# Kernel optimization log

Measured on AMD Instinct MI355X. Metric: run time of the kernel, lower is better.

Reference implementation:

```python
import jax, jax.numpy as jnp
import numpy as np

N_NODES = 100000
N_EDGES = 640000
N_GRAPHS = 2048
HID = 128
L = 3


def setup_inputs() -> dict:
    key = jax.random.key(0)
    ks = jax.random.split(key, 24)
    f32 = jnp.float32
    x = jax.random.normal(ks[0], (N_NODES, 7), dtype=f32)
    edge_attr = jax.random.normal(ks[1], (N_EDGES, 3), dtype=f32)
    edge_index = jax.random.randint(ks[2], (2, N_EDGES), 0, N_NODES, dtype=jnp.int32)
    batch = jnp.sort(jax.random.randint(ks[3], (N_NODES,), 0, N_GRAPHS, dtype=jnp.int32))

    def lin(k, fi, fo):
        return jax.random.normal(k, (fi, fo), dtype=f32) / jnp.sqrt(jnp.asarray(fi, f32))

    inp = dict(x=x, edge_attr=edge_attr, edge_index=edge_index, batch=batch)
    inp["node_w"] = lin(ks[4], 7, HID); inp["node_b"] = jnp.zeros((HID,), f32)
    inp["ew1"] = lin(ks[5], 3, HID);   inp["eb1"] = jnp.zeros((HID,), f32)
    inp["ew2"] = lin(ks[6], HID, HID); inp["eb2"] = jnp.zeros((HID,), f32)
    inp["cw1"] = jnp.stack([lin(ks[7 + i], HID, HID) for i in range(L)])
    inp["cb1"] = jnp.zeros((L, HID), f32)
    inp["cw2"] = jnp.stack([lin(ks[10 + i], HID, HID) for i in range(L)])
    inp["cb2"] = jnp.zeros((L, HID), f32)
    inp["clw1"] = lin(ks[13], HID, 64); inp["clb1"] = jnp.zeros((64,), f32)
    inp["clw2"] = lin(ks[14], 64, 1);   inp["clb2"] = jnp.zeros((1,), f32)
    inp["rw1"] = lin(ks[15], HID, 64);  inp["rb1"] = jnp.zeros((64,), f32)
    inp["rw2"] = lin(ks[16], 64, 1);    inp["rb2"] = jnp.zeros((1,), f32)
    return inp


def reference(x, edge_attr, node_w, node_b, ew1, eb1, ew2, eb2,
              cw1, cb1, cw2, cb2, clw1, clb1, clw2, clb2,
              rw1, rb1, rw2, rb2, edge_index, batch):
    relu = jax.nn.relu
    # encoders
    h = x @ node_w + node_b                                   # [N, H]
    e = relu(edge_attr @ ew1 + eb1) @ ew2 + eb2               # [E, H]
    src, dst = edge_index[0], edge_index[1]
    for l in range(L):
        # GINEConv (eps=0): out = MLP(h_i + sum_j ReLU(h_j + e_ji))
        m = relu(h[src] + e)                                  # [E, H] gather + edge add
        agg = jax.ops.segment_sum(m, dst, num_segments=N_NODES)
        z = h + agg
        h = relu(z @ cw1[l] + cb1[l]) @ cw2[l] + cb2[l]
        h = relu(h)                                           # dropout = identity (eval)
    # global mean pool
    ones = jnp.ones((h.shape[0],), h.dtype)
    counts = jax.ops.segment_sum(ones, batch, num_segments=N_GRAPHS)
    g = jax.ops.segment_sum(h, batch, num_segments=N_GRAPHS) / jnp.maximum(counts, 1.0)[:, None]
    success_logit = (relu(g @ clw1 + clb1) @ clw2 + clb2)[:, 0]
    route_length = (relu(g @ rw1 + rb1) @ rw2 + rb2)[:, 0]
    return success_logit, route_length
```

## Files before the change

### kernel.cpp

```cpp
#include <hip/hip_runtime.h>

#define HID 128
#define LDP 136

typedef short s16x8 __attribute__((ext_vector_type(8)));
typedef float f32x4 __attribute__((ext_vector_type(4)));

__device__ __forceinline__ float bf2f(unsigned int u) {
  union { unsigned int i; float f; } v; v.i = u << 16; return v.f;
}
__device__ __forceinline__ float asf(unsigned int u) {
  union { unsigned int i; float f; } v; v.i = u; return v.f;
}
__device__ __forceinline__ unsigned short f2bf(float f) {
  union { float f; unsigned int i; } v; v.f = f;
  unsigned int r = v.i + 0x7fffu + ((v.i >> 16) & 1u);
  return (unsigned short)(r >> 16);
}

__global__ void k_zero4(float4* __restrict__ p, size_t n4) {
  size_t i = (size_t)blockIdx.x * blockDim.x + threadIdx.x;
  if (i < n4) p[i] = (float4){0.f, 0.f, 0.f, 0.f};
}

__global__ void k_hist(const int* __restrict__ dst, int* __restrict__ deg, int nE) {
  int e = blockIdx.x * blockDim.x + threadIdx.x;
  if (e < nE) atomicAdd(&deg[dst[e]], 1);
}

__global__ void k_scanA(const int* __restrict__ deg, int* __restrict__ bsum) {
  __shared__ int ss[256];
  int t = threadIdx.x;
  ss[t] = deg[blockIdx.x * 256 + t];
  __syncthreads();
  for (int off = 128; off; off >>= 1) {
    if (t < off) ss[t] += ss[t + off];
    __syncthreads();
  }
  if (t == 0) bsum[blockIdx.x] = ss[0];
}

__global__ void k_scanB(const int* __restrict__ bsum, int* __restrict__ bsumx, int NB) {
  __shared__ int sd[512];
  int t = threadIdx.x;
  int v = (t < NB) ? bsum[t] : 0;
  sd[t] = v;
  __syncthreads();
  for (int off = 1; off < 512; off <<= 1) {
    int a = (t >= off) ? sd[t - off] : 0;
    __syncthreads();
    sd[t] += a;
    __syncthreads();
  }
  if (t < NB) bsumx[t] = sd[t] - v;
}

__global__ void k_scanC(const int* __restrict__ deg, const int* __restrict__ bsumx,
                        int* __restrict__ cursor, int* __restrict__ rowptr) {
  __shared__ int ss[256];
  int t = threadIdx.x, i = blockIdx.x * 256 + t;
  int v = deg[i];
  ss[t] = v;
  __syncthreads();
  for (int off = 1; off < 256; off <<= 1) {
    int a = (t >= off) ? ss[t - off] : 0;
    __syncthreads();
    ss[t] += a;
    __syncthreads();
  }
  int ex = ss[t] - v + bsumx[blockIdx.x];
  cursor[i] = ex;
  rowptr[i] = ex;
}

__global__ void k_scatter(const int* __restrict__ src, const int* __restrict__ dst,
                          const float* __restrict__ ea, int* __restrict__ cursor,
                          int* __restrict__ src_s, float* __restrict__ ea_s, int nE) {
  int e = blockIdx.x * blockDim.x + threadIdx.x;
  if (e >= nE) return;
  int d = dst[e];
  int pos = atomicAdd(&cursor[d], 1);
  src_s[pos] = src[e];
  ea_s[(size_t)pos * 3 + 0] = ea[(size_t)e * 3 + 0];
  ea_s[(size_t)pos * 3 + 1] = ea[(size_t)e * 3 + 1];
  ea_s[(size_t)pos * 3 + 2] = ea[(size_t)e * 3 + 2];
}

__global__ void k_prep_w(const float* __restrict__ ew2, const float* __restrict__ cw1,
                         const float* __restrict__ cw2, unsigned short* __restrict__ wT) {
  int idx = blockIdx.x * blockDim.x + threadIdx.x;
  if (idx >= 7 * 16384) return;
  int m = idx >> 14, i = idx & 16383;
  int n = i >> 7, k = i & 127;
  const float* s = (m == 0) ? ew2 : (m <= 3 ? cw1 + (size_t)(m - 1) * 16384
                                            : cw2 + (size_t)(m - 4) * 16384);
  wT[idx] = f2bf(s[k * 128 + n]);
}

__global__ void k_node_enc(const float* __restrict__ x, const float* __restrict__ w,
                           const float* __restrict__ b, unsigned short* __restrict__ h16, int nN) {
  int idx = blockIdx.x * blockDim.x + threadIdx.x;
  if (idx >= nN * HID) return;
  int i = idx >> 7, j = idx & 127;
  float acc = b[j];
  const float* xr = x + (size_t)i * 7;
#pragma unroll
  for (int k = 0; k < 7; ++k) acc += xr[k] * w[k * HID + j];
  h16[idx] = f2bf(acc);
}

__global__ void __launch_bounds__(256) k_edge_gemm(
    const float* __restrict__ ea_s, const float* __restrict__ ew1, const float* __restrict__ eb1,
    const unsigned short* __restrict__ w2t, const float* __restrict__ eb2,
    unsigned short* __restrict__ e16, int nE) {
  __shared__ __attribute__((aligned(16))) unsigned short ts1[128 * LDP];
  __shared__ float eaL[384];
  int tid = threadIdx.x;
  int e0 = blockIdx.x * 128;
  for (int i = tid; i < 384; i += 256) eaL[i] = ea_s[(size_t)e0 * 3 + i];
  __syncthreads();
  {
    int j = tid & 127, r0 = (tid >> 7) * 64;
    float wa = ew1[j], wb = ew1[HID + j], wc = ew1[2 * HID + j], bj = eb1[j];
    for (int r = r0; r < r0 + 64; ++r) {
      float a = bj + eaL[r * 3] * wa + eaL[r * 3 + 1] * wb + eaL[r * 3 + 2] * wc;
      ts1[r * LDP + j] = f2bf(fmaxf(a, 0.f));
    }
  }
  __syncthreads();
  int wave = tid >> 6, lane = tid & 63;
  int l15 = lane & 15, quad = lane >> 4;
  int rbase = (wave >> 1) * 64, nbase = (wave & 1) * 64;
  f32x4 acc[4][4];
#pragma unroll
  for (int i = 0; i < 4; ++i)
#pragma unroll
    for (int j = 0; j < 4; ++j) acc[i][j] = (f32x4){0.f, 0.f, 0.f, 0.f};
  for (int kc = 0; kc < 4; ++kc) {
    int k0 = kc * 32 + quad * 8;
    s16x8 af[4], bf[4];
#pragma unroll
    for (int t = 0; t < 4; ++t)
      af[t] = *(const s16x8*)&ts1[(rbase + t * 16 + l15) * LDP + k0];
#pragma unroll
    for (int t = 0; t < 4; ++t)
      bf[t] = *(const s16x8*)&w2t[(size_t)(nbase + t * 16 + l15) * HID + k0];
#pragma unroll
    for (int i = 0; i < 4; ++i)
#pragma unroll
      for (int j = 0; j < 4; ++j)
        acc[i][j] = __builtin_amdgcn_mfma_f32_16x16x32_bf16(af[i], bf[j], acc[i][j], 0, 0, 0);
  }
  float ebv[4];
#pragma unroll
  for (int t = 0; t < 4; ++t) ebv[t] = eb2[nbase + t * 16 + l15];
#pragma unroll
  for (int tr = 0; tr < 4; ++tr)
#pragma unroll
    for (int reg = 0; reg < 4; ++reg) {
      int row = rbase + tr * 16 + quad * 4 + reg;
#pragma unroll
      for (int tc = 0; tc < 4; ++tc) {
        int col = nbase + tc * 16 + l15;
        e16[(size_t)(e0 + row) * HID + col] = f2bf(acc[tr][tc][reg] + ebv[tc]);
      }
    }
}

__global__ void __launch_bounds__(256) k_conv_csr(
    const unsigned short* __restrict__ h16in, const unsigned short* __restrict__ e16,
    const int* __restrict__ src_s, const int* __restrict__ rowptr,
    const unsigned short* __restrict__ w1t, const float* __restrict__ b1,
    const unsigned short* __restrict__ w2t, const float* __restrict__ b2,
    unsigned short* __restrict__ h16out, int nN) {
  __shared__ __attribute__((aligned(16))) unsigned short zs[64 * LDP];
  __shared__ int rpS[4][20];
  int tid = threadIdx.x;
  int n0 = blockIdx.x * 64;
  int wave = tid >> 6, lane = tid & 63;
  {
    int c2 = lane * 2;
    int wbase = wave * 16;
    int nodeBase = n0 + wbase;
    int nCnt = nN - nodeBase; if (nCnt > 16) nCnt = 16; if (nCnt < 0) nCnt = 0;
#pragma unroll
    for (int i = 0; i < 16; ++i) {
      int n = nodeBase + i;
      unsigned int hv = 0u;
      if (n < nN) hv = *(const unsigned int*)&h16in[(size_t)n * HID + c2];
      *(unsigned int*)&zs[(wbase + i) * LDP + c2] = hv;
    }
    if (lane < 17) {
      int i = (lane < nCnt) ? lane : nCnt;
      rpS[wave][lane] = (nCnt > 0) ? rowptr[nodeBase + i] : 0;
    }
    int eBeg = rpS[wave][0];
    int eEnd = rpS[wave][16];
    if (nCnt > 0 && eBeg < eEnd) {
      float a0 = 0.f, a1 = 0.f;
      int ni = 0;
      int rpEnd = rpS[wave][1];
      int sv0[8], sv1[8];
      unsigned int ev0[8], hv0[8], ev1[8], hv1[8];

#define LOAD_S(svv, base)                                            \
  _Pragma("unroll")                                                  \
  for (int i = 0; i < 8; ++i) {                                      \
    int ix = (base) + i; if (ix >= eEnd) ix = eEnd - 1;              \
    svv[i] = src_s[ix];                                              \
  }
#define LOAD_EH(evv, hvv, svv, base)                                 \
  _Pragma("unroll")                                                  \
  for (int i = 0; i < 8; ++i) {                                      \
    int ix = (base) + i; if (ix >= eEnd) ix = eEnd - 1;              \
    evv[i] = *(const unsigned int*)&e16[(size_t)ix * HID + c2];      \
    hvv[i] = *(const unsigned int*)&h16in[(size_t)svv[i] * HID + c2];\
  }
#define FLUSH()                                                      \
  { int row = wbase + ni;                                            \
    unsigned int z = *(const unsigned int*)&zs[row * LDP + c2];      \
    float z0 = asf(z << 16) + a0, z1 = asf(z & 0xffff0000u) + a1;    \
    *(unsigned int*)&zs[row * LDP + c2] =                            \
        (unsigned int)f2bf(z0) | ((unsigned int)f2bf(z1) << 16);     \
    a0 = 0.f; a1 = 0.f; }
#define FOLD(evv, hvv, base)                                         \
  { int cnt = eEnd - (base); if (cnt > 8) cnt = 8;                   \
    _Pragma("unroll")                                                \
    for (int i = 0; i < 8; ++i) if (i < cnt) {                       \
      int eg = (base) + i;                                           \
      while (eg >= rpEnd) { FLUSH(); ++ni; rpEnd = rpS[wave][ni + 1]; } \
      a0 += fmaxf(asf(hvv[i] << 16) + asf(evv[i] << 16), 0.f);       \
      a1 += fmaxf(asf(hvv[i] & 0xffff0000u) + asf(evv[i] & 0xffff0000u), 0.f); \
    } }

      LOAD_S(sv0, eBeg)
      LOAD_S(sv1, eBeg + 8)
      LOAD_EH(ev0, hv0, sv0, eBeg)
      for (int e = eBeg; e < eEnd; e += 16) {
        if (e + 16 < eEnd) LOAD_S(sv0, e + 16)
        if (e + 8 < eEnd)  LOAD_EH(ev1, hv1, sv1, e + 8)
        FOLD(ev0, hv0, e)
        if (e + 8 < eEnd) {
          if (e + 24 < eEnd) LOAD_S(sv1, e + 24)
          if (e + 16 < eEnd) LOAD_EH(ev0, hv0, sv0, e + 16)
          FOLD(ev1, hv1, e + 8)
        }
      }
      FLUSH()
#undef LOAD_S
#undef LOAD_EH
#undef FLUSH
#undef FOLD
    }
  }
  __syncthreads();
  int l15 = lane & 15, quad = lane >> 4;
  int rbase = (wave >> 1) * 32, nbase = (wave & 1) * 64;
  f32x4 acc[2][4];
#pragma unroll
  for (int i = 0; i < 2; ++i)
#pragma unroll
    for (int j = 0; j < 4; ++j) acc[i][j] = (f32x4){0.f, 0.f, 0.f, 0.f};
  for (int kc = 0; kc < 4; ++kc) {
    int k0 = kc * 32 + quad * 8;
    s16x8 af[2], bf[4];
#pragma unroll
    for (int t = 0; t < 2; ++t)
      af[t] = *(const s16x8*)&zs[(rbase + t * 16 + l15) * LDP + k0];
#pragma unroll
    for (int t = 0; t < 4; ++t)
      bf[t] = *(const s16x8*)&w1t[(size_t)(nbase + t * 16 + l15) * HID + k0];
#pragma unroll
    for (int i = 0; i < 2; ++i)
#pragma unroll
      for (int j = 0; j < 4; ++j)
        acc[i][j] = __builtin_amdgcn_mfma_f32_16x16x32_bf16(af[i], bf[j], acc[i][j], 0, 0, 0);
  }
  __syncthreads();
  {
    float bv[4];
#pragma unroll
    for (int t = 0; t < 4; ++t) bv[t] = b1[nbase + t * 16 + l15];
#pragma unroll
    for (int tr = 0; tr < 2; ++tr)
#pragma unroll
      for (int tc = 0; tc < 4; ++tc)
#pragma unroll
        for (int reg = 0; reg < 4; ++reg) {
          int row = rbase + tr * 16 + quad * 4 + reg;
          int col = nbase + tc * 16 + l15;
          zs[row * LDP + col] = f2bf(fmaxf(acc[tr][tc][reg] + bv[tc], 0.f));
        }
  }
  __syncthreads();
#pragma unroll
  for (int i = 0; i < 2; ++i)
#pragma unroll
    for (int j = 0; j < 4; ++j) acc[i][j] = (f32x4){0.f, 0.f, 0.f, 0.f};
  for (int kc = 0; kc < 4; ++kc) {
    int k0 = kc * 32 + quad * 8;
    s16x8 af[2], bf[4];
#pragma unroll
    for (int t = 0; t < 2; ++t)
      af[t] = *(const s16x8*)&zs[(rbase + t * 16 + l15) * LDP + k0];
#pragma unroll
    for (int t = 0; t < 4; ++t)
      bf[t] = *(const s16x8*)&w2t[(size_t)(nbase + t * 16 + l15) * HID + k0];
#pragma unroll
    for (int i = 0; i < 2; ++i)
#pragma unroll
      for (int j = 0; j < 4; ++j)
        acc[i][j] = __builtin_amdgcn_mfma_f32_16x16x32_bf16(af[i], bf[j], acc[i][j], 0, 0, 0);
  }
  {
    float bv[4];
#pragma unroll
    for (int t = 0; t < 4; ++t) bv[t] = b2[nbase + t * 16 + l15];
#pragma unroll
    for (int tr = 0; tr < 2; ++tr)
#pragma unroll
      for (int reg = 0; reg < 4; ++reg) {
        int grow = n0 + rbase + tr * 16 + quad * 4 + reg;
        if (grow < nN) {
#pragma unroll
          for (int tc = 0; tc < 4; ++tc) {
            int col = nbase + tc * 16 + l15;
            h16out[(size_t)grow * HID + col] = f2bf(fmaxf(acc[tr][tc][reg] + bv[tc], 0.f));
          }
        }
      }
  }
}

__global__ void k_counts(const int* __restrict__ batch, int* __restrict__ cnts, int nN) {
  int i = blockIdx.x * blockDim.x + threadIdx.x;
  if (i < nN) atomicAdd(&cnts[batch[i]], 1);
}

__global__ void __launch_bounds__(256) k_pool2(
    const unsigned short* __restrict__ h16, const int* __restrict__ batch,
    float* __restrict__ g, int nN) {
  __shared__ int bL[128];
  int tid = threadIdx.x;
  int n0 = blockIdx.x * 128;
  if (tid < 128) {
    int n = n0 + tid;
    bL[tid] = (n < nN) ? batch[n] : -1;
  }
  __syncthreads();
  int half = tid >> 7, col = tid & 127;
  int rs = half * 64;
  int cur = -1;
  float s = 0.f;
  for (int r = rs; r < rs + 64; ++r) {
    int b = bL[r];
    float v = (b >= 0) ? bf2f((unsigned int)h16[(size_t)(n0 + r) * HID + col]) : 0.f;
    if (b != cur) {
      if (cur >= 0) atomicAdd(&g[(size_t)cur * HID + col], s);
      cur = b; s = v;
    } else s += v;
  }
  if (cur >= 0) atomicAdd(&g[(size_t)cur * HID + col], s);
}

__global__ void __launch_bounds__(128) k_head(
    const float* __restrict__ g, const int* __restrict__ counts,
    const float* __restrict__ clw1, const float* __restrict__ clb1,
    const float* __restrict__ clw2, const float* __restrict__ clb2,
    const float* __restrict__ rw1, const float* __restrict__ rb1,
    const float* __restrict__ rw2, const float* __restrict__ rb2,
    float* __restrict__ out, int nG) {
  __shared__ float gs[HID];
  int b = blockIdx.x;
  int tid = threadIdx.x;
  float cnt = fmaxf((float)counts[b], 1.f);
  gs[tid] = g[b * HID + tid] / cnt;
  __syncthreads();
  int wave = tid >> 6, lane = tid & 63;
  const float* w1 = wave ? rw1 : clw1;
  const float* b1 = wave ? rb1 : clb1;
  const float* w2 = wave ? rw2 : clw2;
  const float* b2 = wave ? rb2 : clb2;
  float acc = b1[lane];
  for (int k = 0; k < HID; ++k) acc += gs[k] * w1[k * 64 + lane];
  acc = fmaxf(acc, 0.f) * w2[lane];
#pragma unroll
  for (int off = 32; off; off >>= 1) acc += __shfl_down(acc, off);
  if (lane == 0) out[wave * nG + b] = acc + b2[0];
}

extern "C" void kernel_launch(void* const* d_in, const int* in_sizes, int n_in,
                              void* d_out, int out_size, void* d_ws, size_t ws_size,
                              hipStream_t stream) {
  const float* x      = (const float*)d_in[0];
  const float* ea     = (const float*)d_in[1];
  const int*   eidx   = (const int*)d_in[2];
  const int*   batch  = (const int*)d_in[3];
  const float* node_w = (const float*)d_in[4];
  const float* node_b = (const float*)d_in[5];
  const float* ew1    = (const float*)d_in[6];
  const float* eb1    = (const float*)d_in[7];
  const float* ew2    = (const float*)d_in[8];
  const float* eb2    = (const float*)d_in[9];
  const float* cw1    = (const float*)d_in[10];
  const float* cb1    = (const float*)d_in[11];
  const float* cw2    = (const float*)d_in[12];
  const float* cb2    = (const float*)d_in[13];
  const float* clw1   = (const float*)d_in[14];
  const float* clb1   = (const float*)d_in[15];
  const float* clw2   = (const float*)d_in[16];
  const float* clb2   = (const float*)d_in[17];
  const float* rw1    = (const float*)d_in[18];
  const float* rb1    = (const float*)d_in[19];
  const float* rw2    = (const float*)d_in[20];
  const float* rb2    = (const float*)d_in[21];
  float* out = (float*)d_out;

  int nN = in_sizes[3];
  int nE = in_sizes[2] / 2;
  int nG = out_size / 2;
  const int* src = eidx;
  const int* dst = eidx + nE;

  int NB = (nN + 255) / 256;
  int bins = NB * 256;

  size_t hN = (size_t)nN * HID;
  size_t gN = (size_t)nG * HID;
  float* g    = (float*)d_ws;
  int*   cnts = (int*)(g + gN);
  unsigned short* wT   = (unsigned short*)(cnts + nG);
  unsigned short* h16a = wT + 7 * 16384;
  unsigned short* h16b = h16a + hN;
  int* deg    = (int*)(h16b + hN);
  int* cursor = deg + bins;
  int* rowptr = cursor + bins;
  int* bsum   = rowptr + bins;
  int* bsumx  = bsum + 512;
  int* src_s  = bsumx + 512;
  float* ea_s = (float*)(src_s + nE);
  unsigned short* e16 = (unsigned short*)(ea_s + (size_t)3 * nE);

  k_zero4<<<(int)((bins / 4 + 255) / 256), 256, 0, stream>>>((float4*)deg, bins / 4);
  k_hist<<<(nE + 255) / 256, 256, 0, stream>>>(dst, deg, nE);
  k_scanA<<<NB, 256, 0, stream>>>(deg, bsum);
  k_scanB<<<1, 512, 0, stream>>>(bsum, bsumx, NB);
  k_scanC<<<NB, 256, 0, stream>>>(deg, bsumx, cursor, rowptr);
  k_scatter<<<(nE + 255) / 256, 256, 0, stream>>>(src, dst, ea, cursor, src_s, ea_s, nE);

  k_prep_w<<<(7 * 16384 + 255) / 256, 256, 0, stream>>>(ew2, cw1, cw2, wT);
  k_edge_gemm<<<nE / 128, 256, 0, stream>>>(ea_s, ew1, eb1, wT, eb2, e16, nE);
  k_node_enc<<<(nN * HID + 255) / 256, 256, 0, stream>>>(x, node_w, node_b, h16a, nN);

  unsigned short* hin  = h16a;
  unsigned short* hout = h16b;
  for (int l = 0; l < 3; ++l) {
    k_conv_csr<<<(nN + 63) / 64, 256, 0, stream>>>(
        hin, e16, src_s, rowptr,
        wT + (size_t)(1 + l) * 16384, cb1 + (size_t)l * HID,
        wT + (size_t)(4 + l) * 16384, cb2 + (size_t)l * HID, hout, nN);
    unsigned short* t = hin; hin = hout; hout = t;
  }

  k_zero4<<<(int)(((gN + nG) / 4 + 255) / 256), 256, 0, stream>>>((float4*)g, (gN + nG) / 4);
  k_counts<<<(nN + 255) / 256, 256, 0, stream>>>(batch, cnts, nN);
  k_pool2<<<(nN + 127) / 128, 256, 0, stream>>>(hin, batch, g, nN);
  k_head<<<nG, 128, 0, stream>>>(g, cnts, clw1, clb1, clw2, clb2,
                                 rw1, rb1, rw2, rb2, out, nG);
}
```

Measured before the change: 665.6 us.

## Store edge embeddings in 8-edge interleaved chunks and gather edge attrs by index

The scatter kernel now writes only a permutation index instead of copying edge attributes, and the edge GEMM gathers the attributes through that index. The edge GEMM output is staged through shared memory and written in 8-edge chunks, so each lane holds a column pair for 8 consecutive edges and can load them with two 16-byte reads in the conv kernel. The aim is fewer, wider loads of the edge embeddings during the three aggregation passes and less scatter traffic. In exchange it adds an extra LDS round-trip and synchronisation in the edge GEMM, and chunk-aligned iteration with bounds masking in the fold.

```diff
diff --git a/kernel.cpp b/kernel.cpp
--- a/kernel.cpp
+++ b/kernel.cpp
@@ -74,16 +74,14 @@
 }
 
 __global__ void k_scatter(const int* __restrict__ src, const int* __restrict__ dst,
-                          const float* __restrict__ ea, int* __restrict__ cursor,
-                          int* __restrict__ src_s, float* __restrict__ ea_s, int nE) {
+                          int* __restrict__ cursor,
+                          int* __restrict__ src_s, int* __restrict__ esort, int nE) {
   int e = blockIdx.x * blockDim.x + threadIdx.x;
   if (e >= nE) return;
   int d = dst[e];
   int pos = atomicAdd(&cursor[d], 1);
   src_s[pos] = src[e];
-  ea_s[(size_t)pos * 3 + 0] = ea[(size_t)e * 3 + 0];
-  ea_s[(size_t)pos * 3 + 1] = ea[(size_t)e * 3 + 1];
-  ea_s[(size_t)pos * 3 + 2] = ea[(size_t)e * 3 + 2];
+  esort[pos] = e;
 }
 
 __global__ void k_prep_w(const float* __restrict__ ew2, const float* __restrict__ cw1,
@@ -110,14 +108,21 @@
 }
 
 __global__ void __launch_bounds__(256) k_edge_gemm(
-    const float* __restrict__ ea_s, const float* __restrict__ ew1, const float* __restrict__ eb1,
+    const float* __restrict__ ea, const int* __restrict__ esort,
+    const float* __restrict__ ew1, const float* __restrict__ eb1,
     const unsigned short* __restrict__ w2t, const float* __restrict__ eb2,
-    unsigned short* __restrict__ e16, int nE) {
+    unsigned short* __restrict__ echunk, int nE) {
   __shared__ __attribute__((aligned(16))) unsigned short ts1[128 * LDP];
   __shared__ float eaL[384];
+  __shared__ int esL[128];
   int tid = threadIdx.x;
   int e0 = blockIdx.x * 128;
-  for (int i = tid; i < 384; i += 256) eaL[i] = ea_s[(size_t)e0 * 3 + i];
+  if (tid < 128) esL[tid] = esort[e0 + tid];
+  __syncthreads();
+  for (int i = tid; i < 384; i += 256) {
+    int r = i / 3, c = i - r * 3;
+    eaL[i] = ea[(size_t)esL[r] * 3 + c];
+  }
   __syncthreads();
   {
     int j = tid & 127, r0 = (tid >> 7) * 64;
@@ -151,24 +156,48 @@
       for (int j = 0; j < 4; ++j)
         acc[i][j] = __builtin_amdgcn_mfma_f32_16x16x32_bf16(af[i], bf[j], acc[i][j], 0, 0, 0);
   }
-  float ebv[4];
-#pragma unroll
-  for (int t = 0; t < 4; ++t) ebv[t] = eb2[nbase + t * 16 + l15];
-#pragma unroll
-  for (int tr = 0; tr < 4; ++tr)
-#pragma unroll
-    for (int reg = 0; reg < 4; ++reg) {
-      int row = rbase + tr * 16 + quad * 4 + reg;
-#pragma unroll
-      for (int tc = 0; tc < 4; ++tc) {
-        int col = nbase + tc * 16 + l15;
-        e16[(size_t)(e0 + row) * HID + col] = f2bf(acc[tr][tc][reg] + ebv[tc]);
+  __syncthreads();
+  {
+    float ebv[4];
+#pragma unroll
+    for (int t = 0; t < 4; ++t) ebv[t] = eb2[nbase + t * 16 + l15];
+#pragma unroll
+    for (int tr = 0; tr < 4; ++tr)
+#pragma unroll
+      for (int reg = 0; reg < 4; ++reg) {
+        int row = rbase + tr * 16 + quad * 4 + reg;
+#pragma unroll
+        for (int tc = 0; tc < 4; ++tc) {
+          int col = nbase + tc * 16 + l15;
+          ts1[row * LDP + col] = f2bf(acc[tr][tc][reg] + ebv[tc]);
+        }
       }
+  }
+  __syncthreads();
+#pragma unroll
+  for (int t = 0; t < 4; ++t) {
+    int idx = t * 256 + tid;
+    int ch = idx >> 6, cp = idx & 63;
+    unsigned int r[8];
+#pragma unroll
+    for (int j = 0; j < 8; ++j)
+      r[j] = *(const unsigned int*)&ts1[(ch * 8 + j) * LDP + cp * 2];
+    uint4 lo, hi;
+    unsigned int* lw = (unsigned int*)&lo;
+    unsigned int* hw = (unsigned int*)&hi;
+#pragma unroll
+    for (int w = 0; w < 4; ++w) {
+      lw[w] = (r[2 * w] & 0xffffu) | (r[2 * w + 1] << 16);
+      hw[w] = (r[2 * w] >> 16) | (r[2 * w + 1] & 0xffff0000u);
     }
+    size_t baseo = ((size_t)(e0 >> 3) + ch) * 1024 + (size_t)cp * 16;
+    *(uint4*)&echunk[baseo] = lo;
+    *(uint4*)&echunk[baseo + 8] = hi;
+  }
 }
 
 __global__ void __launch_bounds__(256) k_conv_csr(
-    const unsigned short* __restrict__ h16in, const unsigned short* __restrict__ e16,
+    const unsigned short* __restrict__ h16in, const unsigned short* __restrict__ echunk,
     const int* __restrict__ src_s, const int* __restrict__ rowptr,
     const unsigned short* __restrict__ w1t, const float* __restrict__ b1,
     const unsigned short* __restrict__ w2t, const float* __restrict__ b2,
@@ -200,55 +229,68 @@
       float a0 = 0.f, a1 = 0.f;
       int ni = 0;
       int rpEnd = rpS[wave][1];
+      int cBeg = eBeg & ~7;
       int sv0[8], sv1[8];
-      unsigned int ev0[8], hv0[8], ev1[8], hv1[8];
-
-#define LOAD_S(svv, base)                                            \
-  _Pragma("unroll")                                                  \
-  for (int i = 0; i < 8; ++i) {                                      \
-    int ix = (base) + i; if (ix >= eEnd) ix = eEnd - 1;              \
-    svv[i] = src_s[ix];                                              \
-  }
-#define LOAD_EH(evv, hvv, svv, base)                                 \
-  _Pragma("unroll")                                                  \
-  for (int i = 0; i < 8; ++i) {                                      \
-    int ix = (base) + i; if (ix >= eEnd) ix = eEnd - 1;              \
-    evv[i] = *(const unsigned int*)&e16[(size_t)ix * HID + c2];      \
-    hvv[i] = *(const unsigned int*)&h16in[(size_t)svv[i] * HID + c2];\
-  }
-#define FLUSH()                                                      \
-  { int row = wbase + ni;                                            \
-    unsigned int z = *(const unsigned int*)&zs[row * LDP + c2];      \
-    float z0 = asf(z << 16) + a0, z1 = asf(z & 0xffff0000u) + a1;    \
-    *(unsigned int*)&zs[row * LDP + c2] =                            \
-        (unsigned int)f2bf(z0) | ((unsigned int)f2bf(z1) << 16);     \
+      uint4 ec0[2], ec1[2];
+      unsigned int hv0[8], hv1[8];
+
+#define LOAD_S(svv, base)                                              \
+  _Pragma("unroll")                                                    \
+  for (int i = 0; i < 8; ++i) {                                        \
+    int ix = (base) + i;                                               \
+    ix = ix < eBeg ? eBeg : (ix >= eEnd ? eEnd - 1 : ix);              \
+    svv[i] = src_s[ix];                                                \
+  }
+#define LOAD_E(ecc, base)                                              \
+  { size_t bo = (size_t)((base) >> 3) * 1024 + (size_t)c2 * 8;         \
+    ecc[0] = *(const uint4*)&echunk[bo];                               \
+    ecc[1] = *(const uint4*)&echunk[bo + 8]; }
+#define LOAD_H(hvv, svv)                                               \
+  _Pragma("unroll")                                                    \
+  for (int i = 0; i < 8; ++i)                                          \
+    hvv[i] = *(const unsigned int*)&h16in[(size_t)svv[i] * HID + c2];
+#define FLUSH()                                                        \
+  { int row = wbase + ni;                                              \
+    unsigned int z = *(const unsigned int*)&zs[row * LDP + c2];        \
+    float z0 = asf(z << 16) + a0, z1 = asf(z & 0xffff0000u) + a1;      \
+    *(unsigned int*)&zs[row * LDP + c2] =                              \
+        (unsigned int)f2bf(z0) | ((unsigned int)f2bf(z1) << 16);       \
     a0 = 0.f; a1 = 0.f; }
-#define FOLD(evv, hvv, base)                                         \
-  { int cnt = eEnd - (base); if (cnt > 8) cnt = 8;                   \
-    _Pragma("unroll")                                                \
-    for (int i = 0; i < 8; ++i) if (i < cnt) {                       \
-      int eg = (base) + i;                                           \
-      while (eg >= rpEnd) { FLUSH(); ++ni; rpEnd = rpS[wave][ni + 1]; } \
-      a0 += fmaxf(asf(hvv[i] << 16) + asf(evv[i] << 16), 0.f);       \
-      a1 += fmaxf(asf(hvv[i] & 0xffff0000u) + asf(evv[i] & 0xffff0000u), 0.f); \
+#define FOLD(ecc, hvv, base)                                           \
+  { const unsigned int* wA = (const unsigned int*)&ecc[0];             \
+    const unsigned int* wB = (const unsigned int*)&ecc[1];             \
+    _Pragma("unroll")                                                  \
+    for (int i = 0; i < 8; ++i) {                                      \
+      int eg = (base) + i;                                             \
+      if (eg >= eBeg && eg < eEnd) {                                   \
+        while (eg >= rpEnd) { FLUSH(); ++ni; rpEnd = rpS[wave][ni + 1]; } \
+        float e0v = (i & 1) ? asf(wA[i >> 1] & 0xffff0000u)            \
+                            : asf(wA[i >> 1] << 16);                   \
+        float e1v = (i & 1) ? asf(wB[i >> 1] & 0xffff0000u)            \
+                            : asf(wB[i >> 1] << 16);                   \
+        a0 += fmaxf(asf(hvv[i] << 16) + e0v, 0.f);                     \
+        a1 += fmaxf(asf(hvv[i] & 0xffff0000u) + e1v, 0.f);             \
+      }                                                                \
     } }
 
-      LOAD_S(sv0, eBeg)
-      LOAD_S(sv1, eBeg + 8)
-      LOAD_EH(ev0, hv0, sv0, eBeg)
-      for (int e = eBeg; e < eEnd; e += 16) {
-        if (e + 16 < eEnd) LOAD_S(sv0, e + 16)
-        if (e + 8 < eEnd)  LOAD_EH(ev1, hv1, sv1, e + 8)
-        FOLD(ev0, hv0, e)
-        if (e + 8 < eEnd) {
-          if (e + 24 < eEnd) LOAD_S(sv1, e + 24)
-          if (e + 16 < eEnd) LOAD_EH(ev0, hv0, sv0, e + 16)
-          FOLD(ev1, hv1, e + 8)
+      LOAD_S(sv0, cBeg)
+      LOAD_S(sv1, cBeg + 8)
+      LOAD_E(ec0, cBeg)
+      LOAD_H(hv0, sv0)
+      for (int base = cBeg; base < eEnd; base += 16) {
+        if (base + 16 < eEnd) LOAD_S(sv0, base + 16)
+        if (base + 8 < eEnd) { LOAD_E(ec1, base + 8) LOAD_H(hv1, sv1) }
+        FOLD(ec0, hv0, base)
+        if (base + 8 < eEnd) {
+          if (base + 24 < eEnd) LOAD_S(sv1, base + 24)
+          if (base + 16 < eEnd) { LOAD_E(ec0, base + 16) LOAD_H(hv0, sv0) }
+          FOLD(ec1, hv1, base + 8)
         }
       }
       FLUSH()
 #undef LOAD_S
-#undef LOAD_EH
+#undef LOAD_E
+#undef LOAD_H
 #undef FLUSH
 #undef FOLD
     }
@@ -438,25 +480,25 @@
   int* bsum   = rowptr + bins;
   int* bsumx  = bsum + 512;
   int* src_s  = bsumx + 512;
-  float* ea_s = (float*)(src_s + nE);
-  unsigned short* e16 = (unsigned short*)(ea_s + (size_t)3 * nE);
+  int* esort  = src_s + nE;
+  unsigned short* echunk = (unsigned short*)(esort + nE);
 
   k_zero4<<<(int)((bins / 4 + 255) / 256), 256, 0, stream>>>((float4*)deg, bins / 4);
   k_hist<<<(nE + 255) / 256, 256, 0, stream>>>(dst, deg, nE);
   k_scanA<<<NB, 256, 0, stream>>>(deg, bsum);
   k_scanB<<<1, 512, 0, stream>>>(bsum, bsumx, NB);
   k_scanC<<<NB, 256, 0, stream>>>(deg, bsumx, cursor, rowptr);
-  k_scatter<<<(nE + 255) / 256, 256, 0, stream>>>(src, dst, ea, cursor, src_s, ea_s, nE);
+  k_scatter<<<(nE + 255) / 256, 256, 0, stream>>>(src, dst, cursor, src_s, esort, nE);
 
   k_prep_w<<<(7 * 16384 + 255) / 256, 256, 0, stream>>>(ew2, cw1, cw2, wT);
-  k_edge_gemm<<<nE / 128, 256, 0, stream>>>(ea_s, ew1, eb1, wT, eb2, e16, nE);
+  k_edge_gemm<<<nE / 128, 256, 0, stream>>>(ea, esort, ew1, eb1, wT, eb2, echunk, nE);
   k_node_enc<<<(nN * HID + 255) / 256, 256, 0, stream>>>(x, node_w, node_b, h16a, nN);
 
   unsigned short* hin  = h16a;
   unsigned short* hout = h16b;
   for (int l = 0; l < 3; ++l) {
     k_conv_csr<<<(nN + 63) / 64, 256, 0, stream>>>(
-        hin, e16, src_s, rowptr,
+        hin, echunk, src_s, rowptr,
         wT + (size_t)(1 + l) * 16384, cb1 + (size_t)l * HID,
         wT + (size_t)(4 + l) * 16384, cb2 + (size_t)l * HID, hout, nN);
     unsigned short* t = hin; hin = hout; hout = t;
```

Result: slower. 683.0 us (+2.6%).
